# Kernel optimization log

Measured on AMD Instinct MI355X. Metric: run time of the kernel, lower is better.

The kernel has to match this reference:

```python
import jax, jax.numpy as jnp
import numpy as np

T, D = 1024, 1024            # tokens, model dim
E, K = 16, 4                 # routed experts, top-k
G, TG = 4, 2                 # expert groups, limited (top) groups
INTER = 512                  # moe_inter_dim
SHARED_INTER = 2 * INTER     # n_shared_experts * moe_inter_dim
ROUTE_SCALE = 2.5
STD = 0.02


def setup_inputs() -> dict:
    key = jax.random.key(0)
    ks = jax.random.split(key, 9)
    return {
        "x": jax.random.normal(ks[0], (T, D), jnp.float32),
        "token_mask": jnp.ones((T,), jnp.bool_),
        "gate_w": jax.random.normal(ks[1], (E, D), jnp.float32) * STD,
        "gate_bias": jnp.zeros((E,), jnp.float32),  # e_score_correction_bias (zero-init)
        "gate_projs": jax.random.normal(ks[2], (E, INTER, D), jnp.float32) * STD,
        "up_projs": jax.random.normal(ks[3], (E, INTER, D), jnp.float32) * STD,
        "down_projs": jax.random.normal(ks[4], (E, D, INTER), jnp.float32) * STD,
        "shared_gate": jax.random.normal(ks[5], (SHARED_INTER, D), jnp.float32) * STD,
        "shared_up": jax.random.normal(ks[6], (SHARED_INTER, D), jnp.float32) * STD,
        "shared_down": jax.random.normal(ks[7], (D, SHARED_INTER), jnp.float32) * STD,
    }


def _route(x, gate_w, gate_bias):
    # sigmoid scoring with e_score_correction_bias + group-limited top-k (DeepSeek-V3 style)
    scores = jax.nn.sigmoid(x @ gate_w.T)                      # [T, E]
    s = (scores + gate_bias).reshape(T, G, E // G)             # bias-corrected, grouped
    group_scores = jax.lax.top_k(s, 2)[0].sum(-1)              # [T, G] sum of top-2 per group
    gidx = jax.lax.top_k(group_scores, TG)[1]                  # [T, TG]
    gmask = jax.nn.one_hot(gidx, G, dtype=s.dtype).sum(1)      # [T, G] selected-group mask
    masked = (s * gmask[:, :, None]).reshape(T, E)
    idx = jax.lax.top_k(masked, K)[1]                          # [T, K] expert indices
    w = jnp.take_along_axis(scores, idx, axis=1)               # gather original (unbiased) scores
    w = w / w.sum(-1, keepdims=True) * ROUTE_SCALE             # sigmoid renorm + route scale
    return w.astype(x.dtype), idx


def reference(x, token_mask, gate_w, gate_bias, gate_projs, up_projs,
              down_projs, shared_gate, shared_up, shared_down):
    w, idx = _route(x, gate_w, gate_bias)
    # dense combine weights [T, E]: combine[t, e] = sum_k w[t, k] * (idx[t, k] == e)
    combine = (jax.nn.one_hot(idx, E, dtype=x.dtype) * w[..., None]).sum(1)

    def body(acc, p):
        gp, up, dp, c = p                                      # per-expert SwiGLU
        inter = jax.nn.silu(x @ gp.T) * (x @ up.T)             # [T, INTER]
        return acc + c[:, None] * (inter @ dp.T), None

    routed, _ = jax.lax.scan(
        body, jnp.zeros_like(x), (gate_projs, up_projs, down_projs, combine.T))
    shared = (jax.nn.silu(x @ shared_gate.T) * (x @ shared_up.T)) @ shared_down.T
    return routed + shared
```

## Files before the change

kernel.cpp:

```cpp
#include <hip/hip_runtime.h>
#include <stdint.h>

#define TTOK 1024
#define DMODEL 1024
#define NEXP 16
#define TOPK 4
#define INTER 512
#define NSHI 1024
#define RSCALE 2.5f

typedef __bf16 bf16;
typedef __bf16 bf16x8 __attribute__((ext_vector_type(8)));
typedef __bf16 bf16x4 __attribute__((ext_vector_type(4)));
typedef float f32x4 __attribute__((ext_vector_type(4)));

#define APLANE 2064
#define BPLANE 1040

#define OFF_GP 0L
#define OFF_UP 8388608L
#define OFF_DP 16777216L
#define OFF_SG 25165824L
#define OFF_SU 26214400L
#define OFF_SD 27262976L
#define WTOT   28311552L

#define LGKM_BAR()                                            \
  do {                                                        \
    asm volatile("s_waitcnt lgkmcnt(0)" ::: "memory");        \
    __builtin_amdgcn_s_barrier();                             \
  } while (0)

#define CV_STRIDE 884736L
__global__ __launch_bounds__(256)
void convert_kernel(const float* __restrict__ s0, const float* __restrict__ s1,
                    const float* __restrict__ s2, const float* __restrict__ s3,
                    const float* __restrict__ s4, const float* __restrict__ s5,
                    bf16* __restrict__ dst) {
  const long j0 = (long)blockIdx.x * 256 + threadIdx.x;
#pragma unroll
  for (int it = 0; it < 4; ++it) {
    const long j = j0 + (long)it * CV_STRIDE;
    const float* src;
    long local;
    if (j < 1048576L)      { src = s0; local = j; }
    else if (j < 2097152L) { src = s1; local = j - 1048576L; }
    else if (j < 3145728L) { src = s2; local = j - 2097152L; }
    else if (j < 3276800L) { src = s3; local = j - 3145728L; }
    else if (j < 3407872L) { src = s4; local = j - 3276800L; }
    else                   { src = s5; local = j - 3407872L; }
    const float4 a = ((const float4*)src)[local * 2];
    const float4 b = ((const float4*)src)[local * 2 + 1];
    bf16x8 o;
    o[0] = (bf16)a.x; o[1] = (bf16)a.y; o[2] = (bf16)a.z; o[3] = (bf16)a.w;
    o[4] = (bf16)b.x; o[5] = (bf16)b.y; o[6] = (bf16)b.z; o[7] = (bf16)b.w;
    ((bf16x8*)dst)[j] = o;
  }
}

__global__ __launch_bounds__(256)
void scores_kernel(const float* __restrict__ x, const float* __restrict__ gw,
                   float* __restrict__ scores, bf16* __restrict__ xbf) {
  __shared__ float gws[16 * 1024];
  const int tid = threadIdx.x;
  const float4* gw4 = (const float4*)gw;
#pragma unroll
  for (int i0 = 0; i0 < 4096; i0 += 256) {
    const int i = i0 + tid;
    const int e = i >> 8;
    const int dq = (i & 255) << 2;
    const int dd = (dq + 4 * e) & 1023;
    ((float4*)gws)[(e << 8) + (dd >> 2)] = gw4[i];
  }
  {
    const long xb = (long)blockIdx.x * 1024;
#pragma unroll
    for (int p = 0; p < 4; ++p) {
      const long j = xb + p * 256 + tid;
      const float4 v = ((const float4*)x)[j];
      bf16x4 o;
      o.x = (bf16)v.x; o.y = (bf16)v.y; o.z = (bf16)v.z; o.w = (bf16)v.w;
      ((bf16x4*)xbf)[j] = o;
    }
  }
  __syncthreads();
  const int kq = tid >> 6;
  const int lane = tid & 63;
  const int tl = lane >> 4;
  const int e = lane & 15;
  const long token = (long)blockIdx.x * 4 + tl;
  float acc = 0.f;
  const int dbase = kq * 256;
#pragma unroll 8
  for (int i = 0; i < 256; i += 4) {
    const int d = dbase + i;
    const float4 xv = *(const float4*)&x[token * DMODEL + d];
    const float4 wv = *(const float4*)&gws[(e << 10) + ((d + 4 * e) & 1023)];
    acc += xv.x * wv.x + xv.y * wv.y + xv.z * wv.z + xv.w * wv.w;
  }
  __syncthreads();
  gws[kq * 64 + lane] = acc;
  __syncthreads();
  if (kq == 0) {
    const float s = gws[lane] + gws[64 + lane] + gws[128 + lane] + gws[192 + lane];
    scores[token * 16 + e] = s;
  }
}

__global__ __launch_bounds__(1024)
void route_kernel(const float* __restrict__ scores, const float* __restrict__ gb,
                  float* __restrict__ tokW, int* __restrict__ slotTok,
                  int* __restrict__ tokSlot, int* __restrict__ offs,
                  int* __restrict__ tileE, int* __restrict__ tileR,
                  int* __restrict__ tileCnt) {
  __shared__ int cnt[NEXP], cur[NEXP];
  const int t = threadIdx.x;
  if (t < NEXP) cnt[t] = 0;
  __syncthreads();
  float sc[NEXP], s[NEXP];
#pragma unroll
  for (int e = 0; e < NEXP; ++e) {
    const float l = scores[t * NEXP + e];
    sc[e] = 1.f / (1.f + expf(-l));
    s[e] = sc[e] + gb[e];
  }
  float gsc[4];
#pragma unroll
  for (int g = 0; g < 4; ++g) {
    const float a = s[4 * g], b = s[4 * g + 1], c = s[4 * g + 2], d = s[4 * g + 3];
    gsc[g] = fmaxf(fmaxf(fmaxf(a + b, a + c), fmaxf(a + d, b + c)),
                   fmaxf(b + d, c + d));
  }
  int g0 = 0;
  for (int g = 1; g < 4; ++g) if (gsc[g] > gsc[g0]) g0 = g;
  int g1 = (g0 == 0) ? 1 : 0;
  for (int g = 0; g < 4; ++g) if (g != g0 && gsc[g] > gsc[g1]) g1 = g;
  float m[NEXP];
#pragma unroll
  for (int e = 0; e < NEXP; ++e) {
    const int g = e >> 2;
    m[e] = (g == g0 || g == g1) ? s[e] : -1.f;
  }
  int idx[TOPK]; float wv[TOPK]; float wsum = 0.f;
  for (int k = 0; k < TOPK; ++k) {
    int am = 0; float best = m[0];
    for (int e2 = 1; e2 < NEXP; ++e2)
      if (m[e2] > best) { best = m[e2]; am = e2; }
    idx[k] = am; wv[k] = sc[am]; wsum += sc[am]; m[am] = -2.f;
  }
#pragma unroll
  for (int k = 0; k < TOPK; ++k) atomicAdd(&cnt[idx[k]], 1);
  __syncthreads();
  if (t == 0) {
    int acc = 0;
#pragma unroll
    for (int e = 0; e < NEXP; ++e) {
      offs[e] = acc; cur[e] = acc; acc += cnt[e];
    }
    offs[NEXP] = acc;
    int tc = 0;
    int roff = 0;
    for (int e = 0; e < NEXP; ++e) {
      const int end = roff + cnt[e];
      for (int r = roff; r < end; r += 128) { tileE[tc] = e; tileR[tc] = r; ++tc; }
      roff = end;
    }
    for (int r = 0; r < TTOK; r += 128) { tileE[tc] = NEXP; tileR[tc] = r; ++tc; }
    tileCnt[0] = tc;
  }
  __syncthreads();
  const float scl = RSCALE / wsum;
#pragma unroll
  for (int k = 0; k < TOPK; ++k) {
    const int slot = atomicAdd(&cur[idx[k]], 1);
    slotTok[slot] = t;
    tokSlot[t * TOPK + k] = slot;
    tokW[t * TOPK + k] = wv[k] * scl;
  }
}

__global__ __launch_bounds__(256, 2)
void gateup_gemm(const bf16* __restrict__ xbf, const int* __restrict__ slotTok,
                 const int* __restrict__ offs, const int* __restrict__ tileE,
                 const int* __restrict__ tileR, const int* __restrict__ tileCnt,
                 const bf16* __restrict__ wbf,
                 bf16* __restrict__ interR, bf16* __restrict__ interS) {
  const int y = blockIdx.y;
  if (y >= tileCnt[0]) return;
  const int e = tileE[y];
  const bool shd = (e == NEXP);
  const int n0 = blockIdx.x * 64;
  if (!shd && n0 >= INTER) return;
  const int rowStart = tileR[y];
  const int rowEnd = shd ? rowStart + 128 : offs[e + 1];
  const bf16* wgp = shd ? wbf + OFF_SG : wbf + OFF_GP + (long)e * INTER * DMODEL;
  const bf16* wup = shd ? wbf + OFF_SU : wbf + OFF_UP + (long)e * INTER * DMODEL;

  __shared__ __attribute__((aligned(16))) char As[8 * APLANE];
  __shared__ __attribute__((aligned(16))) char Bg[8 * BPLANE];
  __shared__ __attribute__((aligned(16))) char Bu[8 * BPLANE];
  __shared__ int tokS[128];

  const int tid = threadIdx.x;
  if (tid < 128) {
    const int r = rowStart + tid;
    tokS[tid] = shd ? r : slotTok[r < rowEnd ? r : rowStart];
  }
  __syncthreads();

  const int arw = tid >> 3;
  const int aoct = tid & 7;
  const bf16* aSrc[4];
#pragma unroll
  for (int p = 0; p < 4; ++p)
    aSrc[p] = xbf + (long)tokS[p * 32 + arw] * DMODEL + aoct * 8;

  const int bu_ = tid >> 7;
  const int u = tid & 127;
  const int brw = u >> 3;
  const int boct = u & 7;
  const bf16* bSrc = (bu_ ? wup : wgp) + (long)(n0 + brw) * DMODEL + boct * 8;
  char* bDst = bu_ ? Bu : Bg;

  const int lane = tid & 63;
  const int wv = tid >> 6;
  const int q = lane >> 4;
  const int l15 = lane & 15;
  const int wm = (wv >> 1) * 64;
  const int wn = (wv & 1) * 32;

  const f32x4 fz = {0.f, 0.f, 0.f, 0.f};
  f32x4 accG[4][2], accU[4][2];
#pragma unroll
  for (int i = 0; i < 4; ++i)
#pragma unroll
    for (int j = 0; j < 2; ++j) { accG[i][j] = fz; accU[i][j] = fz; }

  bf16x8 av[4];
  bf16x8 bv[4];
#pragma unroll
  for (int p = 0; p < 4; ++p) av[p] = *(const bf16x8*)(aSrc[p]);
#pragma unroll
  for (int p = 0; p < 4; ++p)
    bv[p] = *(const bf16x8*)(bSrc + (long)(p * 16) * DMODEL);

  for (int k0 = 0; k0 < DMODEL; k0 += 64) {
    LGKM_BAR();
#pragma unroll
    for (int p = 0; p < 4; ++p)
      *(bf16x8*)(As + aoct * APLANE + (p * 32 + arw) * 16) = av[p];
#pragma unroll
    for (int p = 0; p < 4; ++p)
      *(bf16x8*)(bDst + boct * BPLANE + (p * 16 + brw) * 16) = bv[p];
    const int kn = k0 + 64;
    if (kn < DMODEL) {
#pragma unroll
      for (int p = 0; p < 4; ++p) av[p] = *(const bf16x8*)(aSrc[p] + kn);
#pragma unroll
      for (int p = 0; p < 4; ++p)
        bv[p] = *(const bf16x8*)(bSrc + (long)(p * 16) * DMODEL + kn);
    }
    LGKM_BAR();
#pragma unroll
    for (int kb = 0; kb < 2; ++kb) {
      bf16x8 aF[4];
#pragma unroll
      for (int mi = 0; mi < 4; ++mi)
        aF[mi] = *(const bf16x8*)(As + (4 * kb + q) * APLANE + (wm + 16 * mi + l15) * 16);
#pragma unroll
      for (int ni = 0; ni < 2; ++ni) {
        const int br = wn + 16 * ni + l15;
        const bf16x8 gF = *(const bf16x8*)(Bg + (4 * kb + q) * BPLANE + br * 16);
        const bf16x8 uF = *(const bf16x8*)(Bu + (4 * kb + q) * BPLANE + br * 16);
#pragma unroll
        for (int mi = 0; mi < 4; ++mi) {
          accG[mi][ni] = __builtin_amdgcn_mfma_f32_16x16x32_bf16(aF[mi], gF, accG[mi][ni], 0, 0, 0);
          accU[mi][ni] = __builtin_amdgcn_mfma_f32_16x16x32_bf16(aF[mi], uF, accU[mi][ni], 0, 0, 0);
        }
      }
    }
  }

  bf16* outI = shd ? interS : interR;
  const int ldI = shd ? NSHI : INTER;
#pragma unroll
  for (int mi = 0; mi < 4; ++mi)
#pragma unroll
    for (int r = 0; r < 4; ++r) {
      const int rowLoc = wm + 16 * mi + q * 4 + r;
      const int row = rowStart + rowLoc;
      if (row < rowEnd) {
#pragma unroll
        for (int ni = 0; ni < 2; ++ni) {
          const float gg = accG[mi][ni][r];
          const float uu = accU[mi][ni][r];
          const float sv = gg / (1.f + __expf(-gg)) * uu;
          outI[(long)row * ldI + (n0 + wn + 16 * ni + l15)] = (bf16)sv;
        }
      }
    }
}

__global__ __launch_bounds__(256, 2)
void down_gemm(const bf16* __restrict__ interR, const bf16* __restrict__ interS,
               const int* __restrict__ offs, const int* __restrict__ tileE,
               const int* __restrict__ tileR, const int* __restrict__ tileCnt,
               const bf16* __restrict__ wbf,
               float* __restrict__ dsR, float* __restrict__ dsS) {
  const int y = blockIdx.y;
  if (y >= tileCnt[0]) return;
  const int e = tileE[y];
  const bool shd = (e == NEXP);
  const int n0 = blockIdx.x * 64;
  const int rowStart = tileR[y];
  const int rowEnd = shd ? rowStart + 128 : offs[e + 1];
  const int Kd = shd ? NSHI : INTER;
  const bf16* A = shd ? interS : interR;
  const bf16* wd = shd ? wbf + OFF_SD : wbf + OFF_DP + (long)e * DMODEL * INTER;

  __shared__ __attribute__((aligned(16))) char As[8 * APLANE];
  __shared__ __attribute__((aligned(16))) char Bs[8 * BPLANE];

  const int tid = threadIdx.x;
  const int arw = tid >> 3;
  const int aoct = tid & 7;
  const bf16* aSrc[4];
#pragma unroll
  for (int p = 0; p < 4; ++p)
    aSrc[p] = A + (long)(rowStart + p * 32 + arw) * Kd + aoct * 8;

  const int brw = tid >> 3;
  const int boct = tid & 7;
  const bf16* bSrc = wd + (long)(n0 + brw) * Kd + boct * 8;

  const int lane = tid & 63;
  const int wv = tid >> 6;
  const int q = lane >> 4;
  const int l15 = lane & 15;
  const int wm = (wv >> 1) * 64;
  const int wn = (wv & 1) * 32;

  const f32x4 fz = {0.f, 0.f, 0.f, 0.f};
  f32x4 acc[4][2];
#pragma unroll
  for (int i = 0; i < 4; ++i)
#pragma unroll
    for (int j = 0; j < 2; ++j) acc[i][j] = fz;

  bf16x8 av[4];
  bf16x8 bv[2];
#pragma unroll
  for (int p = 0; p < 4; ++p) av[p] = *(const bf16x8*)(aSrc[p]);
#pragma unroll
  for (int p = 0; p < 2; ++p)
    bv[p] = *(const bf16x8*)(bSrc + (long)(p * 32) * Kd);

  for (int k0 = 0; k0 < Kd; k0 += 64) {
    LGKM_BAR();
#pragma unroll
    for (int p = 0; p < 4; ++p)
      *(bf16x8*)(As + aoct * APLANE + (p * 32 + arw) * 16) = av[p];
#pragma unroll
    for (int p = 0; p < 2; ++p)
      *(bf16x8*)(Bs + boct * BPLANE + (p * 32 + brw) * 16) = bv[p];
    const int kn = k0 + 64;
    if (kn < Kd) {
#pragma unroll
      for (int p = 0; p < 4; ++p) av[p] = *(const bf16x8*)(aSrc[p] + kn);
#pragma unroll
      for (int p = 0; p < 2; ++p)
        bv[p] = *(const bf16x8*)(bSrc + (long)(p * 32) * Kd + kn);
    }
    LGKM_BAR();
#pragma unroll
    for (int kb = 0; kb < 2; ++kb) {
      bf16x8 aF[4];
#pragma unroll
      for (int mi = 0; mi < 4; ++mi)
        aF[mi] = *(const bf16x8*)(As + (4 * kb + q) * APLANE + (wm + 16 * mi + l15) * 16);
#pragma unroll
      for (int ni = 0; ni < 2; ++ni) {
        const bf16x8 bF = *(const bf16x8*)(Bs + (4 * kb + q) * BPLANE + (wn + 16 * ni + l15) * 16);
#pragma unroll
        for (int mi = 0; mi < 4; ++mi)
          acc[mi][ni] = __builtin_amdgcn_mfma_f32_16x16x32_bf16(aF[mi], bF, acc[mi][ni], 0, 0, 0);
      }
    }
  }

  float* dst = shd ? dsS : dsR;
#pragma unroll
  for (int mi = 0; mi < 4; ++mi)
#pragma unroll
    for (int r = 0; r < 4; ++r) {
      const int rowLoc = wm + 16 * mi + q * 4 + r;
      const int row = rowStart + rowLoc;
      if (row < rowEnd) {
#pragma unroll
        for (int ni = 0; ni < 2; ++ni)
          dst[(long)row * DMODEL + (n0 + wn + 16 * ni + l15)] = acc[mi][ni][r];
      }
    }
}

__global__ __launch_bounds__(256)
void combine_kernel(const float* __restrict__ dsR, const float* __restrict__ dsS,
                    const int* __restrict__ tokSlot, const float* __restrict__ tokW,
                    float* __restrict__ out) {
  const int t = blockIdx.x;
  const int j = threadIdx.x;
  float4 v = ((const float4*)(dsS + (long)t * DMODEL))[j];
#pragma unroll
  for (int k = 0; k < TOPK; ++k) {
    const int s = tokSlot[t * TOPK + k];
    const float w = tokW[t * TOPK + k];
    const float4 r = ((const float4*)(dsR + (long)s * DMODEL))[j];
    v.x += w * r.x; v.y += w * r.y; v.z += w * r.z; v.w += w * r.w;
  }
  ((float4*)(out + (long)t * DMODEL))[j] = v;
}

extern "C" void kernel_launch(void* const* d_in, const int* in_sizes, int n_in,
                              void* d_out, int out_size, void* d_ws, size_t ws_size,
                              hipStream_t stream) {
  const float* x  = (const float*)d_in[0];
  const float* gw = (const float*)d_in[2];
  const float* gb = (const float*)d_in[3];
  const float* gp = (const float*)d_in[4];
  const float* up = (const float*)d_in[5];
  const float* dp = (const float*)d_in[6];
  const float* sg = (const float*)d_in[7];
  const float* su = (const float*)d_in[8];
  const float* sd = (const float*)d_in[9];
  float* out = (float*)d_out;

  char* base = (char*)d_ws;
  size_t off = 0;
  auto alloc = [&](size_t bytes) -> char* {
    off = (off + 255) & ~(size_t)255;
    char* p = base + off;
    off += bytes;
    return p;
  };
  bf16* wbf = (bf16*)alloc((size_t)WTOT * 2);
  bf16* xbf = (bf16*)alloc((size_t)TTOK * DMODEL * 2);
  bf16* interR = (bf16*)alloc((size_t)(TTOK * TOPK + 128) * INTER * 2);
  bf16* interS = (bf16*)alloc((size_t)TTOK * NSHI * 2);
  float* dsR = (float*)alloc((size_t)TTOK * TOPK * DMODEL * 4);
  float* dsS = (float*)alloc((size_t)TTOK * DMODEL * 4);
  float* scores = (float*)alloc((size_t)TTOK * NEXP * 4);
  float* tokW = (float*)alloc(TTOK * TOPK * 4);
  int* slotTok = (int*)alloc(TTOK * TOPK * 4);
  int* tokSlot = (int*)alloc(TTOK * TOPK * 4);
  int* offs = (int*)alloc((NEXP + 1) * 4);
  int* tileE = (int*)alloc(72 * 4);
  int* tileR = (int*)alloc(72 * 4);
  int* tileCnt = (int*)alloc(4);

  convert_kernel<<<3456, 256, 0, stream>>>(gp, up, dp, sg, su, sd, wbf);
  scores_kernel<<<TTOK / 4, 256, 0, stream>>>(x, gw, scores, xbf);
  route_kernel<<<1, 1024, 0, stream>>>(scores, gb, tokW, slotTok, tokSlot,
                                       offs, tileE, tileR, tileCnt);

  gateup_gemm<<<dim3(16, 56, 1), 256, 0, stream>>>(
      xbf, slotTok, offs, tileE, tileR, tileCnt, wbf, interR, interS);
  down_gemm<<<dim3(16, 56, 1), 256, 0, stream>>>(
      interR, interS, offs, tileE, tileR, tileCnt, wbf, dsR, dsS);
  combine_kernel<<<TTOK, 256, 0, stream>>>(dsR, dsS, tokSlot, tokW, out);
}
```

Before: 225.0 us.

## Widen GEMM N tiles to 128 and restructure weight conversion indexing

Both grouped GEMMs now compute 128-column output tiles instead of 64. Each wave holds a 64x64 accumulator block, which halves the grid in x and reuses each gathered A tile across twice as many columns. The convert kernel now handles two contiguous 8-element chunks per thread with twice as many blocks, replacing the strided four-iteration loop. The wider tiles raise register use and shared memory per block (B planes grow to 2064 bytes). With launch bounds of 2 blocks per CU this may cost occupancy or cause spills, and the grid shrinks to fewer blocks.

New measurement: 233.2 us. +3.6%, slower.

```diff
diff --git a/kernel.cpp b/kernel.cpp
--- a/kernel.cpp
+++ b/kernel.cpp
@@ -14,8 +14,7 @@
 typedef __bf16 bf16x4 __attribute__((ext_vector_type(4)));
 typedef float f32x4 __attribute__((ext_vector_type(4)));
 
-#define APLANE 2064
-#define BPLANE 1040
+#define PLANE 2064
 
 #define OFF_GP 0L
 #define OFF_UP 8388608L
@@ -31,31 +30,38 @@
     __builtin_amdgcn_s_barrier();                             \
   } while (0)
 
-#define CV_STRIDE 884736L
 __global__ __launch_bounds__(256)
 void convert_kernel(const float* __restrict__ s0, const float* __restrict__ s1,
                     const float* __restrict__ s2, const float* __restrict__ s3,
                     const float* __restrict__ s4, const float* __restrict__ s5,
                     bf16* __restrict__ dst) {
-  const long j0 = (long)blockIdx.x * 256 + threadIdx.x;
-#pragma unroll
-  for (int it = 0; it < 4; ++it) {
-    const long j = j0 + (long)it * CV_STRIDE;
-    const float* src;
-    long local;
-    if (j < 1048576L)      { src = s0; local = j; }
-    else if (j < 2097152L) { src = s1; local = j - 1048576L; }
-    else if (j < 3145728L) { src = s2; local = j - 2097152L; }
-    else if (j < 3276800L) { src = s3; local = j - 3145728L; }
-    else if (j < 3407872L) { src = s4; local = j - 3276800L; }
-    else                   { src = s5; local = j - 3407872L; }
-    const float4 a = ((const float4*)src)[local * 2];
-    const float4 b = ((const float4*)src)[local * 2 + 1];
-    bf16x8 o;
-    o[0] = (bf16)a.x; o[1] = (bf16)a.y; o[2] = (bf16)a.z; o[3] = (bf16)a.w;
-    o[4] = (bf16)b.x; o[5] = (bf16)b.y; o[6] = (bf16)b.z; o[7] = (bf16)b.w;
-    ((bf16x8*)dst)[j] = o;
-  }
+  const long j0 = (long)blockIdx.x * 512 + threadIdx.x;
+  const long j1 = j0 + 256;
+  const float *srcA, *srcB;
+  long la, lb;
+  if (j0 < 1048576L)      { srcA = s0; la = j0; }
+  else if (j0 < 2097152L) { srcA = s1; la = j0 - 1048576L; }
+  else if (j0 < 3145728L) { srcA = s2; la = j0 - 2097152L; }
+  else if (j0 < 3276800L) { srcA = s3; la = j0 - 3145728L; }
+  else if (j0 < 3407872L) { srcA = s4; la = j0 - 3276800L; }
+  else                    { srcA = s5; la = j0 - 3407872L; }
+  if (j1 < 1048576L)      { srcB = s0; lb = j1; }
+  else if (j1 < 2097152L) { srcB = s1; lb = j1 - 1048576L; }
+  else if (j1 < 3145728L) { srcB = s2; lb = j1 - 2097152L; }
+  else if (j1 < 3276800L) { srcB = s3; lb = j1 - 3145728L; }
+  else if (j1 < 3407872L) { srcB = s4; lb = j1 - 3276800L; }
+  else                    { srcB = s5; lb = j1 - 3407872L; }
+  const float4 a0 = ((const float4*)srcA)[la * 2];
+  const float4 a1 = ((const float4*)srcA)[la * 2 + 1];
+  const float4 b0 = ((const float4*)srcB)[lb * 2];
+  const float4 b1 = ((const float4*)srcB)[lb * 2 + 1];
+  bf16x8 oa, ob;
+  oa[0] = (bf16)a0.x; oa[1] = (bf16)a0.y; oa[2] = (bf16)a0.z; oa[3] = (bf16)a0.w;
+  oa[4] = (bf16)a1.x; oa[5] = (bf16)a1.y; oa[6] = (bf16)a1.z; oa[7] = (bf16)a1.w;
+  ob[0] = (bf16)b0.x; ob[1] = (bf16)b0.y; ob[2] = (bf16)b0.z; ob[3] = (bf16)b0.w;
+  ob[4] = (bf16)b1.x; ob[5] = (bf16)b1.y; ob[6] = (bf16)b1.z; ob[7] = (bf16)b1.w;
+  ((bf16x8*)dst)[j0] = oa;
+  ((bf16x8*)dst)[j1] = ob;
 }
 
 __global__ __launch_bounds__(256)
@@ -189,16 +195,16 @@
   if (y >= tileCnt[0]) return;
   const int e = tileE[y];
   const bool shd = (e == NEXP);
-  const int n0 = blockIdx.x * 64;
+  const int n0 = blockIdx.x * 128;
   if (!shd && n0 >= INTER) return;
   const int rowStart = tileR[y];
   const int rowEnd = shd ? rowStart + 128 : offs[e + 1];
   const bf16* wgp = shd ? wbf + OFF_SG : wbf + OFF_GP + (long)e * INTER * DMODEL;
   const bf16* wup = shd ? wbf + OFF_SU : wbf + OFF_UP + (long)e * INTER * DMODEL;
 
-  __shared__ __attribute__((aligned(16))) char As[8 * APLANE];
-  __shared__ __attribute__((aligned(16))) char Bg[8 * BPLANE];
-  __shared__ __attribute__((aligned(16))) char Bu[8 * BPLANE];
+  __shared__ __attribute__((aligned(16))) char As[8 * PLANE];
+  __shared__ __attribute__((aligned(16))) char Bg[8 * PLANE];
+  __shared__ __attribute__((aligned(16))) char Bu[8 * PLANE];
   __shared__ int tokS[128];
 
   const int tid = threadIdx.x;
@@ -227,37 +233,37 @@
   const int q = lane >> 4;
   const int l15 = lane & 15;
   const int wm = (wv >> 1) * 64;
-  const int wn = (wv & 1) * 32;
+  const int wn = (wv & 1) * 64;
 
   const f32x4 fz = {0.f, 0.f, 0.f, 0.f};
-  f32x4 accG[4][2], accU[4][2];
+  f32x4 accG[4][4], accU[4][4];
 #pragma unroll
   for (int i = 0; i < 4; ++i)
 #pragma unroll
-    for (int j = 0; j < 2; ++j) { accG[i][j] = fz; accU[i][j] = fz; }
+    for (int j = 0; j < 4; ++j) { accG[i][j] = fz; accU[i][j] = fz; }
 
   bf16x8 av[4];
-  bf16x8 bv[4];
+  bf16x8 bv[8];
 #pragma unroll
   for (int p = 0; p < 4; ++p) av[p] = *(const bf16x8*)(aSrc[p]);
 #pragma unroll
-  for (int p = 0; p < 4; ++p)
+  for (int p = 0; p < 8; ++p)
     bv[p] = *(const bf16x8*)(bSrc + (long)(p * 16) * DMODEL);
 
   for (int k0 = 0; k0 < DMODEL; k0 += 64) {
     LGKM_BAR();
 #pragma unroll
     for (int p = 0; p < 4; ++p)
-      *(bf16x8*)(As + aoct * APLANE + (p * 32 + arw) * 16) = av[p];
-#pragma unroll
-    for (int p = 0; p < 4; ++p)
-      *(bf16x8*)(bDst + boct * BPLANE + (p * 16 + brw) * 16) = bv[p];
+      *(bf16x8*)(As + aoct * PLANE + (p * 32 + arw) * 16) = av[p];
+#pragma unroll
+    for (int p = 0; p < 8; ++p)
+      *(bf16x8*)(bDst + boct * PLANE + (p * 16 + brw) * 16) = bv[p];
     const int kn = k0 + 64;
     if (kn < DMODEL) {
 #pragma unroll
       for (int p = 0; p < 4; ++p) av[p] = *(const bf16x8*)(aSrc[p] + kn);
 #pragma unroll
-      for (int p = 0; p < 4; ++p)
+      for (int p = 0; p < 8; ++p)
         bv[p] = *(const bf16x8*)(bSrc + (long)(p * 16) * DMODEL + kn);
     }
     LGKM_BAR();
@@ -266,12 +272,12 @@
       bf16x8 aF[4];
 #pragma unroll
       for (int mi = 0; mi < 4; ++mi)
-        aF[mi] = *(const bf16x8*)(As + (4 * kb + q) * APLANE + (wm + 16 * mi + l15) * 16);
-#pragma unroll
-      for (int ni = 0; ni < 2; ++ni) {
+        aF[mi] = *(const bf16x8*)(As + (4 * kb + q) * PLANE + (wm + 16 * mi + l15) * 16);
+#pragma unroll
+      for (int ni = 0; ni < 4; ++ni) {
         const int br = wn + 16 * ni + l15;
-        const bf16x8 gF = *(const bf16x8*)(Bg + (4 * kb + q) * BPLANE + br * 16);
-        const bf16x8 uF = *(const bf16x8*)(Bu + (4 * kb + q) * BPLANE + br * 16);
+        const bf16x8 gF = *(const bf16x8*)(Bg + (4 * kb + q) * PLANE + br * 16);
+        const bf16x8 uF = *(const bf16x8*)(Bu + (4 * kb + q) * PLANE + br * 16);
 #pragma unroll
         for (int mi = 0; mi < 4; ++mi) {
           accG[mi][ni] = __builtin_amdgcn_mfma_f32_16x16x32_bf16(aF[mi], gF, accG[mi][ni], 0, 0, 0);
@@ -291,7 +297,7 @@
       const int row = rowStart + rowLoc;
       if (row < rowEnd) {
 #pragma unroll
-        for (int ni = 0; ni < 2; ++ni) {
+        for (int ni = 0; ni < 4; ++ni) {
           const float gg = accG[mi][ni][r];
           const float uu = accU[mi][ni][r];
           const float sv = gg / (1.f + __expf(-gg)) * uu;
@@ -311,15 +317,15 @@
   if (y >= tileCnt[0]) return;
   const int e = tileE[y];
   const bool shd = (e == NEXP);
-  const int n0 = blockIdx.x * 64;
+  const int n0 = blockIdx.x * 128;
   const int rowStart = tileR[y];
   const int rowEnd = shd ? rowStart + 128 : offs[e + 1];
   const int Kd = shd ? NSHI : INTER;
   const bf16* A = shd ? interS : interR;
   const bf16* wd = shd ? wbf + OFF_SD : wbf + OFF_DP + (long)e * DMODEL * INTER;
 
-  __shared__ __attribute__((aligned(16))) char As[8 * APLANE];
-  __shared__ __attribute__((aligned(16))) char Bs[8 * BPLANE];
+  __shared__ __attribute__((aligned(16))) char As[8 * PLANE];
+  __shared__ __attribute__((aligned(16))) char Bs[8 * PLANE];
 
   const int tid = threadIdx.x;
   const int arw = tid >> 3;
@@ -338,37 +344,37 @@
   const int q = lane >> 4;
   const int l15 = lane & 15;
   const int wm = (wv >> 1) * 64;
-  const int wn = (wv & 1) * 32;
+  const int wn = (wv & 1) * 64;
 
   const f32x4 fz = {0.f, 0.f, 0.f, 0.f};
-  f32x4 acc[4][2];
+  f32x4 acc[4][4];
 #pragma unroll
   for (int i = 0; i < 4; ++i)
 #pragma unroll
-    for (int j = 0; j < 2; ++j) acc[i][j] = fz;
+    for (int j = 0; j < 4; ++j) acc[i][j] = fz;
 
   bf16x8 av[4];
-  bf16x8 bv[2];
+  bf16x8 bv[4];
 #pragma unroll
   for (int p = 0; p < 4; ++p) av[p] = *(const bf16x8*)(aSrc[p]);
 #pragma unroll
-  for (int p = 0; p < 2; ++p)
+  for (int p = 0; p < 4; ++p)
     bv[p] = *(const bf16x8*)(bSrc + (long)(p * 32) * Kd);
 
   for (int k0 = 0; k0 < Kd; k0 += 64) {
     LGKM_BAR();
 #pragma unroll
     for (int p = 0; p < 4; ++p)
-      *(bf16x8*)(As + aoct * APLANE + (p * 32 + arw) * 16) = av[p];
-#pragma unroll
-    for (int p = 0; p < 2; ++p)
-      *(bf16x8*)(Bs + boct * BPLANE + (p * 32 + brw) * 16) = bv[p];
+      *(bf16x8*)(As + aoct * PLANE + (p * 32 + arw) * 16) = av[p];
+#pragma unroll
+    for (int p = 0; p < 4; ++p)
+      *(bf16x8*)(Bs + boct * PLANE + (p * 32 + brw) * 16) = bv[p];
     const int kn = k0 + 64;
     if (kn < Kd) {
 #pragma unroll
       for (int p = 0; p < 4; ++p) av[p] = *(const bf16x8*)(aSrc[p] + kn);
 #pragma unroll
-      for (int p = 0; p < 2; ++p)
+      for (int p = 0; p < 4; ++p)
         bv[p] = *(const bf16x8*)(bSrc + (long)(p * 32) * Kd + kn);
     }
     LGKM_BAR();
@@ -377,10 +383,10 @@
       bf16x8 aF[4];
 #pragma unroll
       for (int mi = 0; mi < 4; ++mi)
-        aF[mi] = *(const bf16x8*)(As + (4 * kb + q) * APLANE + (wm + 16 * mi + l15) * 16);
-#pragma unroll
-      for (int ni = 0; ni < 2; ++ni) {
-        const bf16x8 bF = *(const bf16x8*)(Bs + (4 * kb + q) * BPLANE + (wn + 16 * ni + l15) * 16);
+        aF[mi] = *(const bf16x8*)(As + (4 * kb + q) * PLANE + (wm + 16 * mi + l15) * 16);
+#pragma unroll
+      for (int ni = 0; ni < 4; ++ni) {
+        const bf16x8 bF = *(const bf16x8*)(Bs + (4 * kb + q) * PLANE + (wn + 16 * ni + l15) * 16);
 #pragma unroll
         for (int mi = 0; mi < 4; ++mi)
           acc[mi][ni] = __builtin_amdgcn_mfma_f32_16x16x32_bf16(aF[mi], bF, acc[mi][ni], 0, 0, 0);
@@ -397,7 +403,7 @@
       const int row = rowStart + rowLoc;
       if (row < rowEnd) {
 #pragma unroll
-        for (int ni = 0; ni < 2; ++ni)
+        for (int ni = 0; ni < 4; ++ni)
           dst[(long)row * DMODEL + (n0 + wn + 16 * ni + l15)] = acc[mi][ni][r];
       }
     }
@@ -457,14 +463,14 @@
   int* tileR = (int*)alloc(72 * 4);
   int* tileCnt = (int*)alloc(4);
 
-  convert_kernel<<<3456, 256, 0, stream>>>(gp, up, dp, sg, su, sd, wbf);
+  convert_kernel<<<6912, 256, 0, stream>>>(gp, up, dp, sg, su, sd, wbf);
   scores_kernel<<<TTOK / 4, 256, 0, stream>>>(x, gw, scores, xbf);
   route_kernel<<<1, 1024, 0, stream>>>(scores, gb, tokW, slotTok, tokSlot,
                                        offs, tileE, tileR, tileCnt);
 
-  gateup_gemm<<<dim3(16, 56, 1), 256, 0, stream>>>(
+  gateup_gemm<<<dim3(8, 56, 1), 256, 0, stream>>>(
       xbf, slotTok, offs, tileE, tileR, tileCnt, wbf, interR, interS);
-  down_gemm<<<dim3(16, 56, 1), 256, 0, stream>>>(
+  down_gemm<<<dim3(8, 56, 1), 256, 0, stream>>>(
       interR, interS, offs, tileE, tileR, tileCnt, wbf, dsR, dsS);
   combine_kernel<<<TTOK, 256, 0, stream>>>(dsR, dsS, tokSlot, tokW, out);
 }
```
